# Performance work log

Measured on AMD Instinct MI355X. Metric: run time of the kernel, lower is better.

## Reference

```python
import jax, jax.numpy as jnp
import numpy as np

NUM_HEADS = 16
H_SELF = 10  # hardcoded h in forward: first 10 heads self-attend, rest cross-attend
DIM = 1024
HEAD_DIM = DIM // NUM_HEADS
SCALE = HEAD_DIM ** -0.5


def _qkv(x, Wqkv):
    # x: [B, N, C] -> q, k, v each [B, H, N, hd]
    B, N, C = x.shape
    qkv = (x @ Wqkv).reshape(B, N, 3, NUM_HEADS, C // NUM_HEADS).transpose(2, 0, 3, 1, 4)
    return qkv[0], qkv[1], qkv[2]


def _attn(q, k, v):
    # q,k,v: [B, h, N, d]
    scores = jnp.einsum('bhqd,bhkd->bhqk', q, k) * SCALE
    probs = jax.nn.softmax(scores, axis=-1)  # attn_drop_ratio = 0.0
    return jnp.einsum('bhqk,bhkd->bhqd', probs, v)


def _proj(xa, xb, Wproj, bproj):
    # xa: [B, 10, N, d], xb: [B, 6, N, d] -> [B, N, C]
    B = xa.shape[0]
    N = xa.shape[2]
    x = jnp.concatenate([xa, xb], axis=1).transpose(0, 2, 1, 3).reshape(B, N, DIM)
    return x @ Wproj + bproj  # proj_drop_ratio = 0.0


def setup_inputs() -> dict:
    key = jax.random.key(0)
    k0, k1, k2, k3 = jax.random.split(key, 4)
    B, N, C = 16, 577, DIM
    x1 = jax.random.normal(k0, (B, N, C), dtype=jnp.float32)
    x2 = jax.random.normal(k1, (B, N, C), dtype=jnp.float32)
    # nn.Linear(dim, dim*3, bias=False): store as [C, 3C] so y = x @ W
    Wqkv = jax.random.normal(k2, (C, 3 * C), dtype=jnp.float32) * 0.02
    # nn.Linear(dim, dim) has bias by default
    Wproj = jax.random.normal(k3, (C, C), dtype=jnp.float32) * 0.02
    bproj = jnp.zeros((C,), dtype=jnp.float32)
    return {"x1": x1, "x2": x2, "Wqkv": Wqkv, "Wproj": Wproj, "bproj": bproj}


def reference(x1, x2, Wqkv, Wproj, bproj):
    q1, k1, v1 = _qkv(x1, Wqkv)
    q2, k2, v2 = _qkv(x2, Wqkv)
    h = H_SELF
    x11 = _attn(q1[:, :h], k1[:, :h], v1[:, :h])  # self-attn branch of x1
    x12 = _attn(q1[:, h:], k2[:, h:], v2[:, h:])  # cross: q from x1, kv from x2
    x22 = _attn(q2[:, :h], k2[:, :h], v2[:, :h])  # self-attn branch of x2
    x21 = _attn(q2[:, h:], k1[:, h:], v1[:, h:])  # cross: q from x2, kv from x1
    out1 = _proj(x11, x12, Wproj, bproj)
    out2 = _proj(x22, x21, Wproj, bproj)
    return (out1, out2)
```

## Files before the change

### kernel.cpp

```cpp
#include <hip/hip_runtime.h>
#include <hip/hip_bf16.h>
#include <stdint.h>
#include <math.h>

typedef __attribute__((ext_vector_type(8))) short bf16x8;
typedef __attribute__((ext_vector_type(4))) float f32x4;
typedef __attribute__((ext_vector_type(8))) unsigned short ushort8;
typedef __attribute__((ext_vector_type(4))) unsigned int uint4v;
typedef __attribute__((ext_vector_type(2))) unsigned int uint2v;

#define NTOK   9232
#define MROWS  18464
#define MPAD   18560
#define NPADV  640
#define QSCALE 0.18033688011112042f

__device__ __forceinline__ uint16_t f2b(float f) {
  uint32_t u = __builtin_bit_cast(uint32_t, f);
  u += 0x7fffu + ((u >> 16) & 1u);
  return (uint16_t)(u >> 16);
}

__device__ __forceinline__ uint32_t packbf(float lo, float hi) {
  return (uint32_t)f2b(lo) | ((uint32_t)f2b(hi) << 16);
}

__device__ __forceinline__ f32x4 mfma16(bf16x8 a, bf16x8 b, f32x4 c) {
  return __builtin_amdgcn_mfma_f32_16x16x32_bf16(a, b, c, 0, 0, 0);
}

__device__ __forceinline__ void gl_lds16(const void* g, void* l) {
  __builtin_amdgcn_global_load_lds(
      (const __attribute__((address_space(1))) uint32_t*)g,
      (__attribute__((address_space(3))) uint32_t*)l, 16, 0, 0);
}

__global__ void convert_x_kernel(const float* __restrict__ x1,
                                 const float* __restrict__ x2,
                                 uint16_t* __restrict__ Xb) {
  const size_t stride = (size_t)gridDim.x * blockDim.x;
  const size_t total8 = (size_t)MPAD * 1024 / 8;
  for (size_t i = (size_t)blockIdx.x * blockDim.x + threadIdx.x; i < total8; i += stride) {
    const size_t e = i * 8;
    const size_t row = e >> 10;
    ushort8 ov;
    if (row < (size_t)MROWS) {
      const float* src = (row < (size_t)NTOK) ? (x1 + e) : (x2 + (e - (size_t)NTOK * 1024));
      float4 a = *(const float4*)(src);
      float4 b = *(const float4*)(src + 4);
      ov[0] = f2b(a.x); ov[1] = f2b(a.y); ov[2] = f2b(a.z); ov[3] = f2b(a.w);
      ov[4] = f2b(b.x); ov[5] = f2b(b.y); ov[6] = f2b(b.z); ov[7] = f2b(b.w);
    } else {
      ov = (ushort8)0;
    }
    *(ushort8*)(Xb + e) = ov;
  }
}

__global__ void transw_kernel(const float* __restrict__ in, uint16_t* __restrict__ out,
                              int R, int Cc) {
  __shared__ float t[32][33];
  const int r0 = blockIdx.x * 32, c0 = blockIdx.y * 32;
  const int tr = threadIdx.x >> 5, tc = threadIdx.x & 31;
#pragma unroll
  for (int i = 0; i < 4; ++i)
    t[tr + i * 8][tc] = in[(size_t)(r0 + tr + i * 8) * Cc + c0 + tc];
  __syncthreads();
#pragma unroll
  for (int i = 0; i < 4; ++i) {
    const int orow = c0 + tr + i * 8;
    out[(size_t)orow * R + r0 + tc] = f2b(t[tc][tr + i * 8]);
  }
}

__global__ __launch_bounds__(256) void gemm_qkv_kernel(
    const uint16_t* __restrict__ A, const uint16_t* __restrict__ Bt,
    uint16_t* __restrict__ Qb, uint16_t* __restrict__ Kb, uint16_t* __restrict__ Vtb) {
  __shared__ uint16_t As[128 * 32];
  __shared__ uint16_t Bs[128 * 32];
  const int tid = threadIdx.x;
  const int w = tid >> 6, l = tid & 63;
  const int c = l & 15, g = l >> 4;
  const int wgid = blockIdx.x;
  const int work = (wgid & 7) * 435 + (wgid >> 3);
  int bm, bn;
  {
    const int stripe = work / 144;
    if (stripe >= 24) { bm = 144; bn = work - 24 * 144; }
    else {
      const int r2 = work % 144;
      const int st8 = r2 / 48, r3 = r2 % 48;
      bm = stripe * 6 + r3 % 6;
      bn = st8 * 8 + r3 / 6;
    }
  }
  const int wm = w >> 1, wn = w & 1;
  f32x4 acc[4][4] = {};

  const int srow = w * 32 + (l >> 2);
  const int scolB = (l & 3) * 16;
  const char* aG = (const char*)(A + (size_t)bm * 128 * 1024);
  const char* bG = (const char*)(Bt + (size_t)bn * 128 * 1024);
  char* aL0 = (char*)As + srow * 64 + scolB;
  char* aL1 = (char*)As + (srow + 16) * 64 + scolB;
  char* bL0 = (char*)Bs + srow * 64 + scolB;
  char* bL1 = (char*)Bs + (srow + 16) * 64 + scolB;
  const char* aG0 = aG + (size_t)srow * 2048 + scolB;
  const char* aG1 = aG + (size_t)(srow + 16) * 2048 + scolB;
  const char* bG0 = bG + (size_t)srow * 2048 + scolB;
  const char* bG1 = bG + (size_t)(srow + 16) * 2048 + scolB;

  for (int ks = 0; ks < 1024; ks += 32) {
    gl_lds16(aG0 + ks * 2, aL0);
    gl_lds16(aG1 + ks * 2, aL1);
    gl_lds16(bG0 + ks * 2, bL0);
    gl_lds16(bG1 + ks * 2, bL1);
    __syncthreads();
    bf16x8 af[4], bfv[4];
#pragma unroll
    for (int mi = 0; mi < 4; ++mi)
      af[mi] = *(const bf16x8*)((const char*)As + (wm * 64 + mi * 16 + c) * 64 + g * 16);
#pragma unroll
    for (int ni = 0; ni < 4; ++ni)
      bfv[ni] = *(const bf16x8*)((const char*)Bs + (wn * 64 + ni * 16 + c) * 64 + g * 16);
#pragma unroll
    for (int mi = 0; mi < 4; ++mi)
#pragma unroll
      for (int ni = 0; ni < 4; ++ni)
        acc[mi][ni] = mfma16(af[mi], bfv[ni], acc[mi][ni]);
    __syncthreads();
  }

  const int sArea = bn >> 3;
#pragma unroll
  for (int mi = 0; mi < 4; ++mi) {
#pragma unroll
    for (int r = 0; r < 4; ++r) {
      const int R = bm * 128 + wm * 64 + mi * 16 + g * 4 + r;
      if (R >= MROWS) continue;
      const int src = (R >= NTOK) ? 1 : 0;
      const int rr = R - src * NTOK;
      const int bb = rr / 577;
      const int nn = rr - bb * 577;
#pragma unroll
      for (int ni = 0; ni < 4; ++ni) {
        const int C = bn * 128 + wn * 64 + ni * 16 + c;
        const int c10 = C & 1023;
        const int hh = c10 >> 6, dd = c10 & 63;
        const size_t bh = ((size_t)src * 16 + bb) * 16 + hh;
        const float v = acc[mi][ni][r];
        if (sArea == 0)
          Qb[(bh * 577 + nn) * 64 + dd] = f2b(v * QSCALE);
        else if (sArea == 1)
          Kb[(bh * 577 + nn) * 64 + dd] = f2b(v);
        else
          Vtb[(bh * 64 + dd) * NPADV + nn] = f2b(v);
      }
    }
  }
}

#define KVB 64
#define ATT_NT 10
__global__ __launch_bounds__(256, 2) void attn_kernel(
    const uint16_t* __restrict__ Qb, const uint16_t* __restrict__ Kb,
    const uint16_t* __restrict__ Vtb, uint16_t* __restrict__ O) {
  __shared__ __align__(128) char smem[65536];
  const int tid = threadIdx.x;
  const int w = tid >> 6, l = tid & 63;
  const int c = l & 15, g = l >> 4;
  const int bid = blockIdx.x;
  const int qc = bid % 3;
  const int p = bid / 3;
  const int h = p & 15, b = (p >> 4) & 15, o = p >> 8;
  const int kvsrc = (h < 10) ? o : (1 - o);
  const uint16_t* qp = Qb + (((size_t)o * 16 + b) * 16 + h) * 577 * 64;
  const uint16_t* kp = Kb + (((size_t)kvsrc * 16 + b) * 16 + h) * 577 * 64;
  const uint16_t* vp = Vtb + (((size_t)kvsrc * 16 + b) * 16 + h) * 64 * NPADV;

  const int qbase = qc * 256 + w * 64;
  const bool active = (qbase <= 576);

  const int sub = l >> 3;
  const int colEl = (((l & 7) ^ sub) << 3);
  char* KsA = smem;
  char* VsA = smem + 16384;
  char* Pb  = smem + 32768 + w * 8192;
  const int rs = (c & 7) << 4;

  bf16x8 Qf[4][2];
  if (active) {
#pragma unroll
    for (int qt = 0; qt < 4; ++qt) {
      const int qrow = min(qbase + qt * 16 + c, 576);
      const uint16_t* qr = qp + (size_t)qrow * 64 + g * 8;
      Qf[qt][0] = *(const bf16x8*)(qr);
      Qf[qt][1] = *(const bf16x8*)(qr + 32);
    }
  }

  f32x4 acc[4][4] = {};
  float m_run[4] = {-3.0e38f, -3.0e38f, -3.0e38f, -3.0e38f};
  float l_run[4] = {0.f, 0.f, 0.f, 0.f};

  auto STAGE = [&](int buf, int kv0) {
#pragma unroll
    for (int i = 0; i < 2; ++i) {
      const int j = w * 2 + i;
      const int row = j * 8 + sub;
      const int gk = min(kv0 + row, 576);
      gl_lds16(kp + (size_t)gk * 64 + colEl, KsA + buf * 8192 + j * 1024 + l * 16);
      gl_lds16(vp + (size_t)row * NPADV + kv0 + colEl, VsA + buf * 8192 + j * 1024 + l * 16);
    }
  };

  STAGE(0, 0);
  __syncthreads();

  for (int t = 0; t < ATT_NT; ++t) {
    if (t < ATT_NT - 1) STAGE((t + 1) & 1, (t + 1) * KVB);
    if (active) {
      const char* Kt = KsA + (t & 1) * 8192;
      const char* Vt = VsA + (t & 1) * 8192;
      bf16x8 Kf[4][2];
#pragma unroll
      for (int kt = 0; kt < 4; ++kt) {
        const char* kr = Kt + (kt * 16 + c) * 128;
        Kf[kt][0] = *(const bf16x8*)(kr + ((g * 16) ^ rs));
        Kf[kt][1] = *(const bf16x8*)(kr + ((64 + g * 16) ^ rs));
      }
      float alpha_[4];
#pragma unroll
      for (int qt = 0; qt < 4; ++qt) {
        f32x4 s[4];
#pragma unroll
        for (int kt = 0; kt < 4; ++kt) {
          f32x4 z = {0.f, 0.f, 0.f, 0.f};
          z = mfma16(Kf[kt][0], Qf[qt][0], z);
          z = mfma16(Kf[kt][1], Qf[qt][1], z);
          s[kt] = z;
        }
        if (t == ATT_NT - 1) {
#pragma unroll
          for (int kt = 0; kt < 4; ++kt)
#pragma unroll
            for (int r = 0; r < 4; ++r) {
              if (kt == 0 && r == 0) { if (g > 0) s[kt][r] = -3.0e38f; }
              else s[kt][r] = -3.0e38f;
            }
        }
        float mt = s[0][0];
#pragma unroll
        for (int kt = 0; kt < 4; ++kt)
#pragma unroll
          for (int r = 0; r < 4; ++r) mt = fmaxf(mt, s[kt][r]);
        mt = fmaxf(mt, __shfl_xor(mt, 16));
        mt = fmaxf(mt, __shfl_xor(mt, 32));
        const float mnew = fmaxf(m_run[qt], mt);
        const float al = exp2f(m_run[qt] - mnew);
        m_run[qt] = mnew;
        alpha_[qt] = al;
        float lt = 0.f;
#pragma unroll
        for (int kt = 0; kt < 4; ++kt)
#pragma unroll
          for (int r = 0; r < 4; ++r) {
            const float pv = exp2f(s[kt][r] - mnew);
            s[kt][r] = pv;
            lt += pv;
          }
        lt += __shfl_xor(lt, 16);
        lt += __shfl_xor(lt, 32);
        l_run[qt] = l_run[qt] * al + lt;
        const int rowOff = (qt * 16 + c) * 128;
#pragma unroll
        for (int kt = 0; kt < 4; ++kt) {
          const uint2v pw = {packbf(s[kt][0], s[kt][1]), packbf(s[kt][2], s[kt][3])};
          *(uint2v*)(Pb + rowOff + ((kt * 32 + g * 8) ^ rs)) = pw;
        }
      }
#pragma unroll
      for (int dt = 0; dt < 4; ++dt)
#pragma unroll
        for (int qt = 0; qt < 4; ++qt)
#pragma unroll
          for (int r = 0; r < 4; ++r) acc[dt][qt][r] *= alpha_[qt];
      bf16x8 pf[4][2];
#pragma unroll
      for (int qt = 0; qt < 4; ++qt) {
        const char* pr = Pb + (qt * 16 + c) * 128;
        pf[qt][0] = *(const bf16x8*)(pr + ((g * 16) ^ rs));
        pf[qt][1] = *(const bf16x8*)(pr + ((64 + g * 16) ^ rs));
      }
#pragma unroll
      for (int dt = 0; dt < 4; ++dt) {
        const char* vr = Vt + (dt * 16 + c) * 128;
        const bf16x8 v0 = *(const bf16x8*)(vr + ((g * 16) ^ rs));
        const bf16x8 v1 = *(const bf16x8*)(vr + ((64 + g * 16) ^ rs));
#pragma unroll
        for (int qt = 0; qt < 4; ++qt) {
          acc[dt][qt] = mfma16(v0, pf[qt][0], acc[dt][qt]);
          acc[dt][qt] = mfma16(v1, pf[qt][1], acc[dt][qt]);
        }
      }
    }
    __syncthreads();
  }

  if (active) {
#pragma unroll
    for (int qt = 0; qt < 4; ++qt) {
      const float inv = 1.0f / l_run[qt];
      const int rowOff = (qt * 16 + c) * 128;
#pragma unroll
      for (int dt = 0; dt < 4; ++dt) {
        const uint2v pw = {packbf(acc[dt][qt][0] * inv, acc[dt][qt][1] * inv),
                           packbf(acc[dt][qt][2] * inv, acc[dt][qt][3] * inv)};
        *(uint2v*)(Pb + rowOff + ((dt * 32 + g * 8) ^ rs)) = pw;
      }
    }
    const size_t obase = ((size_t)o * NTOK + (size_t)b * 577) * 1024 + h * 64;
#pragma unroll
    for (int pass = 0; pass < 8; ++pass) {
      const int row = pass * 8 + (l >> 3);
      const int tok = qbase + row;
      const uint4v vv = *(const uint4v*)(Pb + row * 128 + (((l & 7) * 16) ^ ((row & 7) << 4)));
      if (tok <= 576)
        *(uint4v*)(O + obase + (size_t)tok * 1024 + (l & 7) * 8) = vv;
    }
  }
}

__global__ __launch_bounds__(256) void gemm_proj_kernel(
    const uint16_t* __restrict__ A, const uint16_t* __restrict__ Bt,
    const float* __restrict__ bias, float* __restrict__ out) {
  __shared__ uint16_t As[128 * 32];
  __shared__ uint16_t Bs[128 * 32];
  const int tid = threadIdx.x;
  const int w = tid >> 6, l = tid & 63;
  const int c = l & 15, g = l >> 4;
  const int wgid = blockIdx.x;
  const int work = (wgid & 7) * 145 + (wgid >> 3);
  int bm, bn;
  {
    const int stripe = work / 48;
    if (stripe >= 24) { bm = 144; bn = work - 24 * 48; }
    else { const int r3 = work % 48; bm = stripe * 6 + r3 % 6; bn = r3 / 6; }
  }
  const int wm = w >> 1, wn = w & 1;
  f32x4 acc[4][4] = {};

  const int srow = w * 32 + (l >> 2);
  const int scolB = (l & 3) * 16;
  const char* aG = (const char*)(A + (size_t)bm * 128 * 1024);
  const char* bG = (const char*)(Bt + (size_t)bn * 128 * 1024);
  char* aL0 = (char*)As + srow * 64 + scolB;
  char* aL1 = (char*)As + (srow + 16) * 64 + scolB;
  char* bL0 = (char*)Bs + srow * 64 + scolB;
  char* bL1 = (char*)Bs + (srow + 16) * 64 + scolB;
  const char* aG0 = aG + (size_t)srow * 2048 + scolB;
  const char* aG1 = aG + (size_t)(srow + 16) * 2048 + scolB;
  const char* bG0 = bG + (size_t)srow * 2048 + scolB;
  const char* bG1 = bG + (size_t)(srow + 16) * 2048 + scolB;

  for (int ks = 0; ks < 1024; ks += 32) {
    gl_lds16(aG0 + ks * 2, aL0);
    gl_lds16(aG1 + ks * 2, aL1);
    gl_lds16(bG0 + ks * 2, bL0);
    gl_lds16(bG1 + ks * 2, bL1);
    __syncthreads();
    bf16x8 af[4], bfv[4];
#pragma unroll
    for (int mi = 0; mi < 4; ++mi)
      af[mi] = *(const bf16x8*)((const char*)As + (wm * 64 + mi * 16 + c) * 64 + g * 16);
#pragma unroll
    for (int ni = 0; ni < 4; ++ni)
      bfv[ni] = *(const bf16x8*)((const char*)Bs + (wn * 64 + ni * 16 + c) * 64 + g * 16);
#pragma unroll
    for (int mi = 0; mi < 4; ++mi)
#pragma unroll
      for (int ni = 0; ni < 4; ++ni)
        acc[mi][ni] = mfma16(af[mi], bfv[ni], acc[mi][ni]);
    __syncthreads();
  }

#pragma unroll
  for (int mi = 0; mi < 4; ++mi) {
#pragma unroll
    for (int r = 0; r < 4; ++r) {
      const int R = bm * 128 + wm * 64 + mi * 16 + g * 4 + r;
      if (R >= MROWS) continue;
#pragma unroll
      for (int ni = 0; ni < 4; ++ni) {
        const int C = bn * 128 + wn * 64 + ni * 16 + c;
        out[(size_t)R * 1024 + C] = acc[mi][ni][r] + bias[C];
      }
    }
  }
}

extern "C" void kernel_launch(void* const* d_in, const int* in_sizes, int n_in,
                              void* d_out, int out_size, void* d_ws, size_t ws_size,
                              hipStream_t stream) {
  (void)in_sizes; (void)n_in; (void)out_size; (void)ws_size;
  const float* x1    = (const float*)d_in[0];
  const float* x2    = (const float*)d_in[1];
  const float* Wqkv  = (const float*)d_in[2];
  const float* Wproj = (const float*)d_in[3];
  const float* bproj = (const float*)d_in[4];
  float* out = (float*)d_out;

  char* ws = (char*)d_ws;
  size_t off = 0;
  auto alloc = [&](size_t bytes) -> char* {
    char* p = ws + off;
    off += (bytes + 255) & ~(size_t)255;
    return p;
  };
  uint16_t* Xb     = (uint16_t*)alloc((size_t)MPAD * 1024 * 2);
  uint16_t* Wqkvt  = (uint16_t*)alloc((size_t)3072 * 1024 * 2);
  uint16_t* Wprojt = (uint16_t*)alloc((size_t)1024 * 1024 * 2);
  uint16_t* Qb     = (uint16_t*)alloc((size_t)512 * 577 * 64 * 2);
  uint16_t* Kb     = (uint16_t*)alloc((size_t)512 * 577 * 64 * 2);
  const size_t vtBytes = (size_t)512 * 64 * NPADV * 2;
  uint16_t* Vtb    = (uint16_t*)alloc(vtBytes);

  hipMemsetAsync(Vtb, 0, vtBytes, stream);

  convert_x_kernel<<<2048, 256, 0, stream>>>(x1, x2, Xb);
  transw_kernel<<<dim3(32, 96), 256, 0, stream>>>(Wqkv, Wqkvt, 1024, 3072);
  transw_kernel<<<dim3(32, 32), 256, 0, stream>>>(Wproj, Wprojt, 1024, 1024);
  gemm_qkv_kernel<<<3480, 256, 0, stream>>>(Xb, Wqkvt, Qb, Kb, Vtb);
  attn_kernel<<<1536, 256, 0, stream>>>(Qb, Kb, Vtb, Xb );
  gemm_proj_kernel<<<1160, 256, 0, stream>>>(Xb, Wprojt, bproj, out);
}
```

Before: 424.8 us.

## Double-buffer GEMM K-loop with BK=64, XOR-swizzled LDS and interleaved prefetch

Rewrites the main loop of both the QKV and projection GEMMs. It now uses two LDS buffers with a K tile of 64 instead of 32. Global-to-LDS loads for the next tile are issued between MFMA phases of the current tile, and an XOR swizzle on the LDS layout avoids bank conflicts on fragment reads. The phases use s_setprio and raw barriers, and the launch bounds request 2 blocks per CU. The aim is to hide memory latency and cut LDS conflicts, at the cost of 64KB of LDS per block and barrier/waitcnt ordering that is more fragile.

```diff
diff --git a/kernel.cpp b/kernel.cpp
--- a/kernel.cpp
+++ b/kernel.cpp
@@ -73,13 +73,67 @@
   }
 }
 
-__global__ __launch_bounds__(256) void gemm_qkv_kernel(
+#define GEMM_PHASE(BUF, MIH, KK)                                               \
+  {                                                                            \
+    bf16x8 a0 = LDA(BUF, 2 * (MIH), KK), a1 = LDA(BUF, 2 * (MIH) + 1, KK);     \
+    bf16x8 b0 = LDB(BUF, 0, KK), b1 = LDB(BUF, 1, KK);                         \
+    bf16x8 b2 = LDB(BUF, 2, KK), b3 = LDB(BUF, 3, KK);                         \
+    __builtin_amdgcn_s_barrier();                                              \
+    __builtin_amdgcn_s_setprio(1);                                             \
+    acc[2 * (MIH)][0] = mfma16(a0, b0, acc[2 * (MIH)][0]);                     \
+    acc[2 * (MIH)][1] = mfma16(a0, b1, acc[2 * (MIH)][1]);                     \
+    acc[2 * (MIH)][2] = mfma16(a0, b2, acc[2 * (MIH)][2]);                     \
+    acc[2 * (MIH)][3] = mfma16(a0, b3, acc[2 * (MIH)][3]);                     \
+    acc[2 * (MIH) + 1][0] = mfma16(a1, b0, acc[2 * (MIH) + 1][0]);             \
+    acc[2 * (MIH) + 1][1] = mfma16(a1, b1, acc[2 * (MIH) + 1][1]);             \
+    acc[2 * (MIH) + 1][2] = mfma16(a1, b2, acc[2 * (MIH) + 1][2]);             \
+    acc[2 * (MIH) + 1][3] = mfma16(a1, b3, acc[2 * (MIH) + 1][3]);             \
+    __builtin_amdgcn_s_setprio(0);                                             \
+  }
+
+#define GEMM_PHASE3(BUF)                                                       \
+  {                                                                            \
+    bf16x8 a0 = LDA(BUF, 2, 1), a1 = LDA(BUF, 3, 1);                           \
+    bf16x8 b0 = LDB(BUF, 0, 1), b1 = LDB(BUF, 1, 1);                           \
+    bf16x8 b2 = LDB(BUF, 2, 1), b3 = LDB(BUF, 3, 1);                           \
+    asm volatile("s_waitcnt vmcnt(0)" ::: "memory");                           \
+    __builtin_amdgcn_s_barrier();                                              \
+    __builtin_amdgcn_sched_barrier(0);                                         \
+    __builtin_amdgcn_s_setprio(1);                                             \
+    acc[2][0] = mfma16(a0, b0, acc[2][0]);                                     \
+    acc[2][1] = mfma16(a0, b1, acc[2][1]);                                     \
+    acc[2][2] = mfma16(a0, b2, acc[2][2]);                                     \
+    acc[2][3] = mfma16(a0, b3, acc[2][3]);                                     \
+    acc[3][0] = mfma16(a1, b0, acc[3][0]);                                     \
+    acc[3][1] = mfma16(a1, b1, acc[3][1]);                                     \
+    acc[3][2] = mfma16(a1, b2, acc[3][2]);                                     \
+    acc[3][3] = mfma16(a1, b3, acc[3][3]);                                     \
+    __builtin_amdgcn_s_setprio(0);                                             \
+  }
+
+#define GEMM_KLOOP                                                             \
+  for (int q = 0; q < 4; ++q) { SA(0, 0, q); SB(0, 0, q); }                    \
+  asm volatile("s_waitcnt vmcnt(0)" ::: "memory");                             \
+  __builtin_amdgcn_s_barrier();                                                \
+  for (int t = 0; t < 16; ++t) {                                               \
+    const int buf = t & 1, nb = buf ^ 1;                                       \
+    if (t < 15) { SA(nb, t + 1, 0); SB(nb, t + 1, 0);                          \
+                  SA(nb, t + 1, 1); SB(nb, t + 1, 1); }                        \
+    GEMM_PHASE(buf, 0, 0);                                                     \
+    if (t < 15) { SA(nb, t + 1, 2); SB(nb, t + 1, 2);                          \
+                  SA(nb, t + 1, 3); SB(nb, t + 1, 3); }                        \
+    GEMM_PHASE(buf, 0, 1);                                                     \
+    GEMM_PHASE(buf, 1, 0);                                                     \
+    GEMM_PHASE3(buf);                                                          \
+  }
+
+__global__ __launch_bounds__(256, 2) void gemm_qkv_kernel(
     const uint16_t* __restrict__ A, const uint16_t* __restrict__ Bt,
     uint16_t* __restrict__ Qb, uint16_t* __restrict__ Kb, uint16_t* __restrict__ Vtb) {
-  __shared__ uint16_t As[128 * 32];
-  __shared__ uint16_t Bs[128 * 32];
-  const int tid = threadIdx.x;
-  const int w = tid >> 6, l = tid & 63;
+  __shared__ uint16_t As2[2][8192];
+  __shared__ uint16_t Bs2[2][8192];
+  const int tt = threadIdx.x;
+  const int w = tt >> 6, l = tt & 63;
   const int c = l & 15, g = l >> 4;
   const int wgid = blockIdx.x;
   const int work = (wgid & 7) * 435 + (wgid >> 3);
@@ -97,39 +151,33 @@
   const int wm = w >> 1, wn = w & 1;
   f32x4 acc[4][4] = {};
 
-  const int srow = w * 32 + (l >> 2);
-  const int scolB = (l & 3) * 16;
   const char* aG = (const char*)(A + (size_t)bm * 128 * 1024);
   const char* bG = (const char*)(Bt + (size_t)bn * 128 * 1024);
-  char* aL0 = (char*)As + srow * 64 + scolB;
-  char* aL1 = (char*)As + (srow + 16) * 64 + scolB;
-  char* bL0 = (char*)Bs + srow * 64 + scolB;
-  char* bL1 = (char*)Bs + (srow + 16) * 64 + scolB;
-  const char* aG0 = aG + (size_t)srow * 2048 + scolB;
-  const char* aG1 = aG + (size_t)(srow + 16) * 2048 + scolB;
-  const char* bG0 = bG + (size_t)srow * 2048 + scolB;
-  const char* bG1 = bG + (size_t)(srow + 16) * 2048 + scolB;
-
-  for (int ks = 0; ks < 1024; ks += 32) {
-    gl_lds16(aG0 + ks * 2, aL0);
-    gl_lds16(aG1 + ks * 2, aL1);
-    gl_lds16(bG0 + ks * 2, bL0);
-    gl_lds16(bG1 + ks * 2, bL1);
-    __syncthreads();
-    bf16x8 af[4], bfv[4];
-#pragma unroll
-    for (int mi = 0; mi < 4; ++mi)
-      af[mi] = *(const bf16x8*)((const char*)As + (wm * 64 + mi * 16 + c) * 64 + g * 16);
-#pragma unroll
-    for (int ni = 0; ni < 4; ++ni)
-      bfv[ni] = *(const bf16x8*)((const char*)Bs + (wn * 64 + ni * 16 + c) * 64 + g * 16);
-#pragma unroll
-    for (int mi = 0; mi < 4; ++mi)
-#pragma unroll
-      for (int ni = 0; ni < 4; ++ni)
-        acc[mi][ni] = mfma16(af[mi], bfv[ni], acc[mi][ni]);
-    __syncthreads();
-  }
+  const int srow = tt >> 3;
+  const int schunk = tt & 7;
+  const int swc = schunk ^ (srow & 7);
+  const int cr7 = c & 7;
+
+  auto SA = [&](int buf, int t, int q) {
+    const int row = q * 32 + srow;
+    gl_lds16(aG + (size_t)row * 2048 + t * 128 + swc * 16,
+             (uint16_t*)As2 + buf * 8192 + row * 64 + schunk * 8);
+  };
+  auto SB = [&](int buf, int t, int q) {
+    const int row = q * 32 + srow;
+    gl_lds16(bG + (size_t)row * 2048 + t * 128 + swc * 16,
+             (uint16_t*)Bs2 + buf * 8192 + row * 64 + schunk * 8);
+  };
+  auto LDA = [&](int buf, int mi, int kk) -> bf16x8 {
+    return *(const bf16x8*)((const uint16_t*)As2 + buf * 8192 +
+                            (wm * 64 + mi * 16 + c) * 64 + (((kk * 4 + g) ^ cr7) << 3));
+  };
+  auto LDB = [&](int buf, int ni, int kk) -> bf16x8 {
+    return *(const bf16x8*)((const uint16_t*)Bs2 + buf * 8192 +
+                            (wn * 64 + ni * 16 + c) * 64 + (((kk * 4 + g) ^ cr7) << 3));
+  };
+
+  GEMM_KLOOP
 
   const int sArea = bn >> 3;
 #pragma unroll
@@ -331,13 +379,13 @@
   }
 }
 
-__global__ __launch_bounds__(256) void gemm_proj_kernel(
+__global__ __launch_bounds__(256, 2) void gemm_proj_kernel(
     const uint16_t* __restrict__ A, const uint16_t* __restrict__ Bt,
     const float* __restrict__ bias, float* __restrict__ out) {
-  __shared__ uint16_t As[128 * 32];
-  __shared__ uint16_t Bs[128 * 32];
-  const int tid = threadIdx.x;
-  const int w = tid >> 6, l = tid & 63;
+  __shared__ uint16_t As2[2][8192];
+  __shared__ uint16_t Bs2[2][8192];
+  const int tt = threadIdx.x;
+  const int w = tt >> 6, l = tt & 63;
   const int c = l & 15, g = l >> 4;
   const int wgid = blockIdx.x;
   const int work = (wgid & 7) * 145 + (wgid >> 3);
@@ -350,39 +398,33 @@
   const int wm = w >> 1, wn = w & 1;
   f32x4 acc[4][4] = {};
 
-  const int srow = w * 32 + (l >> 2);
-  const int scolB = (l & 3) * 16;
   const char* aG = (const char*)(A + (size_t)bm * 128 * 1024);
   const char* bG = (const char*)(Bt + (size_t)bn * 128 * 1024);
-  char* aL0 = (char*)As + srow * 64 + scolB;
-  char* aL1 = (char*)As + (srow + 16) * 64 + scolB;
-  char* bL0 = (char*)Bs + srow * 64 + scolB;
-  char* bL1 = (char*)Bs + (srow + 16) * 64 + scolB;
-  const char* aG0 = aG + (size_t)srow * 2048 + scolB;
-  const char* aG1 = aG + (size_t)(srow + 16) * 2048 + scolB;
-  const char* bG0 = bG + (size_t)srow * 2048 + scolB;
-  const char* bG1 = bG + (size_t)(srow + 16) * 2048 + scolB;
-
-  for (int ks = 0; ks < 1024; ks += 32) {
-    gl_lds16(aG0 + ks * 2, aL0);
-    gl_lds16(aG1 + ks * 2, aL1);
-    gl_lds16(bG0 + ks * 2, bL0);
-    gl_lds16(bG1 + ks * 2, bL1);
-    __syncthreads();
-    bf16x8 af[4], bfv[4];
-#pragma unroll
-    for (int mi = 0; mi < 4; ++mi)
-      af[mi] = *(const bf16x8*)((const char*)As + (wm * 64 + mi * 16 + c) * 64 + g * 16);
-#pragma unroll
-    for (int ni = 0; ni < 4; ++ni)
-      bfv[ni] = *(const bf16x8*)((const char*)Bs + (wn * 64 + ni * 16 + c) * 64 + g * 16);
-#pragma unroll
-    for (int mi = 0; mi < 4; ++mi)
-#pragma unroll
-      for (int ni = 0; ni < 4; ++ni)
-        acc[mi][ni] = mfma16(af[mi], bfv[ni], acc[mi][ni]);
-    __syncthreads();
-  }
+  const int srow = tt >> 3;
+  const int schunk = tt & 7;
+  const int swc = schunk ^ (srow & 7);
+  const int cr7 = c & 7;
+
+  auto SA = [&](int buf, int t, int q) {
+    const int row = q * 32 + srow;
+    gl_lds16(aG + (size_t)row * 2048 + t * 128 + swc * 16,
+             (uint16_t*)As2 + buf * 8192 + row * 64 + schunk * 8);
+  };
+  auto SB = [&](int buf, int t, int q) {
+    const int row = q * 32 + srow;
+    gl_lds16(bG + (size_t)row * 2048 + t * 128 + swc * 16,
+             (uint16_t*)Bs2 + buf * 8192 + row * 64 + schunk * 8);
+  };
+  auto LDA = [&](int buf, int mi, int kk) -> bf16x8 {
+    return *(const bf16x8*)((const uint16_t*)As2 + buf * 8192 +
+                            (wm * 64 + mi * 16 + c) * 64 + (((kk * 4 + g) ^ cr7) << 3));
+  };
+  auto LDB = [&](int buf, int ni, int kk) -> bf16x8 {
+    return *(const bf16x8*)((const uint16_t*)Bs2 + buf * 8192 +
+                            (wn * 64 + ni * 16 + c) * 64 + (((kk * 4 + g) ^ cr7) << 3));
+  };
+
+  GEMM_KLOOP
 
 #pragma unroll
   for (int mi = 0; mi < 4; ++mi) {
```

After: 444.9 us. 1.05x slower.
